# Kernel optimization log

Measured on AMD Instinct MI355X. Metric: run time of the kernel, lower is better.

## Reference

```python
import jax, jax.numpy as jnp
import numpy as np

SHIFT = 1  # (random.random() > 0.5) * 2 - 1 fixed to +1


def setup_inputs() -> dict:
    key = jax.random.key(0)
    k1, k2 = jax.random.split(key)
    x = jax.random.normal(k1, (1, 256, 14, 14), dtype=jnp.float32)
    w = jax.random.normal(k2, (256, 3, 3, 128), dtype=jnp.float32)  # learned param
    return {"x": x, "w": w}


def reference(x, w):
    s = SHIFT
    # 'ilkj -> ikjl': (1,256,14,14) -> (1,14,14,256)
    t = jnp.transpose(x, (0, 2, 3, 1))
    t = jnp.roll(t, s, axis=2)
    # unfold kernel (3,1), pad (1,0): treat axis1 as C=14, axis2 as H=14, axis3 as W=256.
    # Result layout (N, C, kh, H, W) matches torch's (1,14,3,14,256) reshape.
    tp = jnp.pad(t, ((0, 0), (0, 0), (1, 1), (0, 0)))
    t = jnp.stack([tp[:, :, a:a + 14, :] for a in range(3)], axis=2)  # (1,14,3,14,256)
    # split 256 -> (14,2,128) merged as 28, roll, split back, sum pair
    t = t.reshape(1, 14, 3, 28, 128)
    t = jnp.roll(t, s, axis=3)
    t = t.reshape(1, 14, 3, 14, 2, 128).sum(axis=4)  # (1,14,3,14,128)
    # second unfold (3,1), pad (1,0): here C=1, H=14 (axis1), W=3*14*128 flattened.
    tp = jnp.pad(t, ((0, 0), (1, 1), (0, 0), (0, 0), (0, 0)))
    t3 = jnp.stack([tp[:, a:a + 14] for a in range(3)], axis=1)  # (1,3,14,3,14,128)
    # contraction: m=1, j=3, n=14, k=3, o=14, l=128 ; w: (i=256, j=3, k=3, l=128)
    y = jnp.einsum('mjnkol,ijkl->mino', t3, w)  # (1,256,14,14)
    return y
```

## Files before the change

### kernel.cpp

```cpp
#include <hip/hip_runtime.h>
#include <hip/hip_bf16.h>


#define PSTR 64

__global__ __launch_bounds__(512) void fused_shiftconv(
    const float* __restrict__ x,
    const float* __restrict__ w,
    float* __restrict__ out)
{
    __shared__ __align__(16) float rs[126 * 128];
    __shared__ __align__(16) float parts[224 * PSTR];

    const int n    = blockIdx.x;
    const int ig   = blockIdx.y;
    const int t    = threadIdx.x;
    const int lane = t & 63;
    const int wv   = t >> 6;

    const float* wbase = w + (ig * 16 + wv * 2) * 1152;
    float4 wq[2][4];
    float2 wt[2];
    #pragma unroll
    for (int ii = 0; ii < 2; ++ii) {
        const float* wp = wbase + ii * 1152;
        #pragma unroll
        for (int qi = 0; qi < 4; ++qi)
            wq[ii][qi] = *(const float4*)(wp + qi * 256 + lane * 4);
        wt[ii] = *(const float2*)(wp + 1024 + lane * 2);
    }

    if (t < 384) {
        const int j = t >> 7;
        const int l = t & 127;
        const int h = n + j - 1;
        float xlo[14], xhi[14];
        if ((unsigned)h < 14u) {
            const float* p0 = x + l * 196 + h * 14;
            const float* p1 = x + (128 + l) * 196 + h * 14;
            #pragma unroll
            for (int wi = 0; wi < 14; wi += 2) {
                float2 a = *(const float2*)(p0 + wi);
                float2 b = *(const float2*)(p1 + wi);
                xlo[wi] = a.x; xlo[wi + 1] = a.y;
                xhi[wi] = b.x; xhi[wi + 1] = b.y;
            }
        } else {
            #pragma unroll
            for (int wi = 0; wi < 14; ++wi) { xlo[wi] = 0.f; xhi[wi] = 0.f; }
        }
        #pragma unroll
        for (int k = 0; k < 3; ++k) {
            #pragma unroll
            for (int o = 0; o < 14; ++o) {
                float val = 0.f;
                const int wb = o + k - 1;
                if (wb >= 0 && wb < 14) val += xlo[wb ? wb - 1 : 13];
                const int v  = o ? o - 1 : 13;
                const int wa = v + k - 1;
                if (wa >= 0 && wa < 14) val += xhi[wa ? wa - 1 : 13];
                rs[((j * 3 + k) * 14 + o) * 128 + l] = val;
            }
        }
    }
    __syncthreads();

    const int rbl   = (lane & 31) * 4;
    const int jkhi  = lane >> 5;
    const int prow0 = wv * 28;
    #pragma unroll 2
    for (int o = 0; o < 14; ++o) {
        const int ro = o * 128;
        float4 rv0 = *(const float4*)(rs + ((0 * 2 + jkhi) * 14) * 128 + ro + rbl);
        float4 rv1 = *(const float4*)(rs + ((1 * 2 + jkhi) * 14) * 128 + ro + rbl);
        float4 rv2 = *(const float4*)(rs + ((2 * 2 + jkhi) * 14) * 128 + ro + rbl);
        float4 rv3 = *(const float4*)(rs + ((3 * 2 + jkhi) * 14) * 128 + ro + rbl);
        float2 rt  = *(const float2*)(rs + (112 + o) * 128 + lane * 2);
        #pragma unroll
        for (int ii = 0; ii < 2; ++ii) {
            float a0, a1;
            a0  = rv0.x * wq[ii][0].x + rv0.y * wq[ii][0].y + rv0.z * wq[ii][0].z + rv0.w * wq[ii][0].w;
            a1  = rv1.x * wq[ii][1].x + rv1.y * wq[ii][1].y + rv1.z * wq[ii][1].z + rv1.w * wq[ii][1].w;
            a0 += rv2.x * wq[ii][2].x + rv2.y * wq[ii][2].y + rv2.z * wq[ii][2].z + rv2.w * wq[ii][2].w;
            a1 += rv3.x * wq[ii][3].x + rv3.y * wq[ii][3].y + rv3.z * wq[ii][3].z + rv3.w * wq[ii][3].w;
            a0 += rt.x * wt[ii].x + rt.y * wt[ii].y;
            const int row = prow0 + ii * 14 + o;
            parts[row * PSTR + ((lane + 4 * row) & 63)] = a0 + a1;
        }
    }
    __syncthreads();

    if (t < 224) {
        const float* pr = parts + t * PSTR;
        float s0 = 0.f, s1 = 0.f;
        #pragma unroll
        for (int g = 0; g < 16; g += 2) {
            float4 v0 = *(const float4*)(pr + ((4 * g + 4 * t) & 63));
            float4 v1 = *(const float4*)(pr + ((4 * (g + 1) + 4 * t) & 63));
            s0 += v0.x + v0.y + v0.z + v0.w;
            s1 += v1.x + v1.y + v1.z + v1.w;
        }
        const int wv2 = t / 28;
        const int rem = t - wv2 * 28;
        const int ii  = rem / 14;
        const int o   = rem - ii * 14;
        const int i   = ig * 16 + wv2 * 2 + ii;
        out[(i * 14 + n) * 14 + o] = s0 + s1;
    }
}

extern "C" void kernel_launch(void* const* d_in, const int* in_sizes, int n_in,
                              void* d_out, int out_size, void* d_ws, size_t ws_size,
                              hipStream_t stream) {
    const float* x = (const float*)d_in[0];
    const float* w = (const float*)d_in[1];
    float* out = (float*)d_out;
    dim3 grid(14, 16);
    fused_shiftconv<<<grid, 512, 0, stream>>>(x, w, out);
}
```

Before: 60.71 us.

## Replace LDS partial-sum reduction with DPP wave reduction and regrid work split

Each wave now reduces its per-lane partial dot products with a DPP-based 64-lane sum and lane 63 writes the result, which removes the shared-memory parts buffer, the second barrier and the tail reduction pass. The grid changes to split output columns into two halves and give each wave four output channels instead of two. The block count stays the same, but each block computes 7 columns for 32 channels. The cost is more weight registers per thread, a serial DPP chain per channel, and rs staging that is duplicated across the two column halves.

```diff
diff --git a/kernel.cpp b/kernel.cpp
--- a/kernel.cpp
+++ b/kernel.cpp
@@ -2,7 +2,25 @@
 #include <hip/hip_bf16.h>
 
 
-#define PSTR 64
+__device__ __forceinline__ float __uint_as_float_(unsigned int u) {
+    union { unsigned int i; float f; } c; c.i = u; return c.f;
+}
+
+template<int CTRL, int RM>
+__device__ __forceinline__ float dpp_add(float v) {
+    int moved = __builtin_amdgcn_update_dpp(0, __float_as_int(v), CTRL, RM, 0xf, true);
+    return v + __int_as_float(moved);
+}
+
+__device__ __forceinline__ float wave_sum64(float v) {
+    v = dpp_add<0x111, 0xf>(v);
+    v = dpp_add<0x112, 0xf>(v);
+    v = dpp_add<0x114, 0xf>(v);
+    v = dpp_add<0x118, 0xf>(v);
+    v = dpp_add<0x142, 0xa>(v);
+    v = dpp_add<0x143, 0xc>(v);
+    return v;
+}
 
 __global__ __launch_bounds__(512) void fused_shiftconv(
     const float* __restrict__ x,
@@ -10,20 +28,20 @@
     float* __restrict__ out)
 {
     __shared__ __align__(16) float rs[126 * 128];
-    __shared__ __align__(16) float parts[224 * PSTR];
 
     const int n    = blockIdx.x;
-    const int ig   = blockIdx.y;
+    const int os   = blockIdx.y;
+    const int ig   = blockIdx.z;
     const int t    = threadIdx.x;
     const int lane = t & 63;
     const int wv   = t >> 6;
 
-    const float* wbase = w + (ig * 16 + wv * 2) * 1152;
-    float4 wq[2][4];
-    float2 wt[2];
+    const int ibase = ig * 32 + wv * 4;
+    float4 wq[4][4];
+    float2 wt[4];
     #pragma unroll
-    for (int ii = 0; ii < 2; ++ii) {
-        const float* wp = wbase + ii * 1152;
+    for (int ii = 0; ii < 4; ++ii) {
+        const float* wp = w + (ibase + ii) * 1152;
         #pragma unroll
         for (int qi = 0; qi < 4; ++qi)
             wq[ii][qi] = *(const float4*)(wp + qi * 256 + lane * 4);
@@ -65,47 +83,33 @@
     }
     __syncthreads();
 
-    const int rbl   = (lane & 31) * 4;
-    const int jkhi  = lane >> 5;
-    const int prow0 = wv * 28;
-    #pragma unroll 2
-    for (int o = 0; o < 14; ++o) {
+    const int rbl  = (lane & 31) * 4;
+    const int jkhi = lane >> 5;
+    #pragma unroll
+    for (int oo = 0; oo < 7; ++oo) {
+        const int o  = os * 7 + oo;
         const int ro = o * 128;
-        float4 rv0 = *(const float4*)(rs + ((0 * 2 + jkhi) * 14) * 128 + ro + rbl);
-        float4 rv1 = *(const float4*)(rs + ((1 * 2 + jkhi) * 14) * 128 + ro + rbl);
-        float4 rv2 = *(const float4*)(rs + ((2 * 2 + jkhi) * 14) * 128 + ro + rbl);
-        float4 rv3 = *(const float4*)(rs + ((3 * 2 + jkhi) * 14) * 128 + ro + rbl);
+        float4 rv0 = *(const float4*)(rs + ((0 + jkhi) * 14) * 128 + ro + rbl);
+        float4 rv1 = *(const float4*)(rs + ((2 + jkhi) * 14) * 128 + ro + rbl);
+        float4 rv2 = *(const float4*)(rs + ((4 + jkhi) * 14) * 128 + ro + rbl);
+        float4 rv3 = *(const float4*)(rs + ((6 + jkhi) * 14) * 128 + ro + rbl);
         float2 rt  = *(const float2*)(rs + (112 + o) * 128 + lane * 2);
+        float s[4];
         #pragma unroll
-        for (int ii = 0; ii < 2; ++ii) {
+        for (int ii = 0; ii < 4; ++ii) {
             float a0, a1;
             a0  = rv0.x * wq[ii][0].x + rv0.y * wq[ii][0].y + rv0.z * wq[ii][0].z + rv0.w * wq[ii][0].w;
             a1  = rv1.x * wq[ii][1].x + rv1.y * wq[ii][1].y + rv1.z * wq[ii][1].z + rv1.w * wq[ii][1].w;
             a0 += rv2.x * wq[ii][2].x + rv2.y * wq[ii][2].y + rv2.z * wq[ii][2].z + rv2.w * wq[ii][2].w;
             a1 += rv3.x * wq[ii][3].x + rv3.y * wq[ii][3].y + rv3.z * wq[ii][3].z + rv3.w * wq[ii][3].w;
             a0 += rt.x * wt[ii].x + rt.y * wt[ii].y;
-            const int row = prow0 + ii * 14 + o;
-            parts[row * PSTR + ((lane + 4 * row) & 63)] = a0 + a1;
+            s[ii] = wave_sum64(a0 + a1);
         }
-    }
-    __syncthreads();
-
-    if (t < 224) {
-        const float* pr = parts + t * PSTR;
-        float s0 = 0.f, s1 = 0.f;
-        #pragma unroll
-        for (int g = 0; g < 16; g += 2) {
-            float4 v0 = *(const float4*)(pr + ((4 * g + 4 * t) & 63));
-            float4 v1 = *(const float4*)(pr + ((4 * (g + 1) + 4 * t) & 63));
-            s0 += v0.x + v0.y + v0.z + v0.w;
-            s1 += v1.x + v1.y + v1.z + v1.w;
+        if (lane == 63) {
+            #pragma unroll
+            for (int ii = 0; ii < 4; ++ii)
+                out[(ibase + ii) * 196 + n * 14 + o] = s[ii];
         }
-        const int wv2 = t / 28;
-        const int rem = t - wv2 * 28;
-        const int ii  = rem / 14;
-        const int o   = rem - ii * 14;
-        const int i   = ig * 16 + wv2 * 2 + ii;
-        out[(i * 14 + n) * 14 + o] = s0 + s1;
     }
 }
 
@@ -115,6 +119,6 @@
     const float* x = (const float*)d_in[0];
     const float* w = (const float*)d_in[1];
     float* out = (float*)d_out;
-    dim3 grid(14, 16);
+    dim3 grid(14, 2, 8);
     fused_shiftconv<<<grid, 512, 0, stream>>>(x, w, out);
 }
```

Measured after the change: 61.67 us. About the same (+1.6%).
